# Kernel tuning notes

Hardware: AMD Instinct MI355X
Metric: run time of the kernel (lower is better)

Reference implementation:

```python
import math
import jax, jax.numpy as jnp
import numpy as np

B, T, D = 2, 2048, 1024
NUM_HEADS = 16
NUM_KV_HEADS = 4
HEAD_DIM = 64
ROPE_THETA = 500000.0


def precompute_freqs_cis(dim, seq_len, theta):
    freqs = 1.0 / theta ** (jnp.arange(0, dim, 2).astype(jnp.float32) / dim)
    freqs = jnp.outer(jnp.arange(seq_len), freqs)  # [T, dim//2]
    return jnp.cos(freqs), jnp.sin(freqs)


def apply_rotary_emb(xq, xk, cos, sin):
    # xq:[B,T,H,Dh], cos/sin:[T,Dh//2] -> broadcast as [1,T,1,Dh//2]
    c = cos[None, :, None, :]
    s = sin[None, :, None, :]

    def rot(x):
        xr = x.reshape(*x.shape[:-1], -1, 2)
        x0, x1 = xr[..., 0], xr[..., 1]
        return jnp.stack([x0 * c - x1 * s, x1 * c + x0 * s], axis=-1).reshape(x.shape)

    return rot(xq), rot(xk)


def setup_inputs() -> dict:
    key = jax.random.key(0)
    ks = jax.random.split(key, 5)
    x = jax.random.normal(ks[0], (B, T, D), dtype=jnp.float32)
    # causal mask [B,1,T,T]
    mask = jnp.broadcast_to(jnp.tril(jnp.ones((T, T), dtype=bool))[None, None], (B, 1, T, T))
    sq = 1.0 / math.sqrt(D)
    Wq = jax.random.normal(ks[1], (D, NUM_HEADS * HEAD_DIM), dtype=jnp.float32) * sq
    Wk = jax.random.normal(ks[2], (D, NUM_KV_HEADS * HEAD_DIM), dtype=jnp.float32) * sq
    Wv = jax.random.normal(ks[3], (D, NUM_KV_HEADS * HEAD_DIM), dtype=jnp.float32) * sq
    Wo = jax.random.normal(ks[4], (NUM_HEADS * HEAD_DIM, D), dtype=jnp.float32) * (1.0 / math.sqrt(NUM_HEADS * HEAD_DIM))
    return {"x": x, "mask": mask, "Wq": Wq, "Wk": Wk, "Wv": Wv, "Wo": Wo}


def reference(x, mask, Wq, Wk, Wv, Wo):
    b, t, _ = x.shape
    n_rep = NUM_HEADS // NUM_KV_HEADS
    q = (x @ Wq).reshape(b, t, NUM_HEADS, HEAD_DIM)
    k = (x @ Wk).reshape(b, t, NUM_KV_HEADS, HEAD_DIM)
    v = (x @ Wv).reshape(b, t, NUM_KV_HEADS, HEAD_DIM)
    cos, sin = precompute_freqs_cis(HEAD_DIM, t, ROPE_THETA)
    q, k = apply_rotary_emb(q, k, cos, sin)
    k = jnp.repeat(k, n_rep, axis=2)
    v = jnp.repeat(v, n_rep, axis=2)
    q = q.transpose(0, 2, 1, 3)  # [B,H,T,Dh]
    k = k.transpose(0, 2, 1, 3)
    v = v.transpose(0, 2, 1, 3)
    scale = 1.0 / math.sqrt(HEAD_DIM)
    attn = jnp.einsum('bhqd,bhkd->bhqk', q, k) * scale
    attn = jnp.where(mask, attn, -1e9)
    attn = jax.nn.softmax(attn, axis=-1)
    out = jnp.einsum('bhqk,bhkd->bhqd', attn, v)
    out = out.transpose(0, 2, 1, 3).reshape(b, t, -1)
    return out @ Wo
```

## Files before the change

### kernel.cpp

```cpp
#include <hip/hip_runtime.h>
#include <hip/hip_bf16.h>

#define B_  2
#define T_  2048
#define D_  1024
#define H_  16
#define KH_ 4
#define DH_ 64

typedef __attribute__((ext_vector_type(8))) short bf16x8;
typedef __attribute__((ext_vector_type(4))) float f32x4;

#define QSCALE 0.18033688011112043f

#if defined(__has_builtin)
#  if __has_builtin(__builtin_amdgcn_exp2f)
#    define EXP2F(x) __builtin_amdgcn_exp2f(x)
#  endif
#endif
#ifndef EXP2F
#  define EXP2F(x) exp2f(x)
#endif

__device__ __forceinline__ unsigned short f2bf(float f) {
  union { float f; unsigned int u; } v; v.f = f;
  return (unsigned short)((v.u + 0x7FFFu + ((v.u >> 16) & 1u)) >> 16);
}
__device__ __forceinline__ unsigned int pk2(float a, float b) {
  union { __hip_bfloat162 h2; unsigned int u; } v;
  v.h2 = __float22bfloat162_rn(make_float2(a, b));
  return v.u;
}

__device__ __forceinline__ void g2l16(const void* g, void* l) {
  __builtin_amdgcn_global_load_lds(
      (const __attribute__((address_space(1))) void*)g,
      (__attribute__((address_space(3))) void*)l, 16, 0, 0);
}


__global__ __launch_bounds__(256) void prep_kernel(
    const float* __restrict__ x,  const float* __restrict__ Wq,
    const float* __restrict__ Wk, const float* __restrict__ Wv,
    const float* __restrict__ Wo,
    short* __restrict__ xb, short* __restrict__ WT, short* __restrict__ WoT,
    float2* __restrict__ tbl) {
  __shared__ short Ts[64 * 72];
  const int bid = blockIdx.x, tid = threadIdx.x;

  if (bid < 2048) {
    const size_t i8 = ((size_t)bid * 256 + tid) * 8;
    const float4 a = *(const float4*)&x[i8];
    const float4 b = *(const float4*)&x[i8 + 4];
    uint4 p; p.x = pk2(a.x, a.y); p.y = pk2(a.z, a.w);
    p.z = pk2(b.x, b.y); p.w = pk2(b.z, b.w);
    *(uint4*)&xb[i8] = p;
  } else if (bid < 2688) {
    const bool isW = bid < 2432;
    const int idx = isW ? (bid - 2048) : (bid - 2432);
    const int n0 = (idx >> 4) * 64, k0 = (idx & 15) * 64;
    const float* src; int ncols, c0; short* dst;
    if (isW) {
      dst = WT;
      if (n0 < 1024)      { src = Wq; ncols = 1024; c0 = n0; }
      else if (n0 < 1280) { src = Wk; ncols = 256;  c0 = n0 - 1024; }
      else                { src = Wv; ncols = 256;  c0 = n0 - 1280; }
    } else { dst = WoT; src = Wo; ncols = 1024; c0 = n0; }
    for (int i = tid; i < 1024; i += 256) {
      const int kr = i >> 4, c4 = (i & 15) << 2;
      const int kc = isW ? kr : ((kr & 15) * 4 + (kr >> 4));
      const float4 w = *(const float4*)&src[(size_t)(k0 + kr) * ncols + c0 + c4];
      Ts[(c4 + 0) * 72 + kc] = (short)f2bf(w.x);
      Ts[(c4 + 1) * 72 + kc] = (short)f2bf(w.y);
      Ts[(c4 + 2) * 72 + kc] = (short)f2bf(w.z);
      Ts[(c4 + 3) * 72 + kc] = (short)f2bf(w.w);
    }
    __syncthreads();
    for (int c = tid; c < 512; c += 256) {
      const int nr = c >> 3, c8 = (c & 7) * 8;
      *(bf16x8*)&dst[(size_t)(n0 + nr) * 1024 + k0 + c8] =
          *(const bf16x8*)&Ts[nr * 72 + c8];
    }
  } else {
    const int e = (bid - 2688) * 256 + tid;
    const int t = e >> 5, i2 = e & 31;
    const float freq = exp2f(-(float)(2 * i2) * (18.931568569324174f / 64.0f));
    float sn, cs; sincosf((float)t * freq, &sn, &cs);
    tbl[e] = make_float2(cs, sn);
  }
}

__global__ __launch_bounds__(256) void qkv_mfma_kernel(
    const short* __restrict__ xb, const short* __restrict__ WT,
    const float2* __restrict__ tbl,
    short* __restrict__ qo, short* __restrict__ ko, short* __restrict__ vt) {
  __shared__ short Xsh[2][128 * 64];
  __shared__ short Wth[2][64 * 64];
  const int tid = threadIdx.x;
  const int lane = tid & 63, w = tid >> 6;
  const int lm = lane & 15, quad = lane >> 4;
  const int bid = blockIdx.x;
  const int xcd = bid & 7, slot = bid >> 3;
  const int m0 = (xcd * 4 + (slot & 3)) * 128;
  const int n0 = (slot >> 2) * 64;

  f32x4 acc[2][4];
  #pragma unroll
  for (int sm = 0; sm < 2; ++sm)
    #pragma unroll
    for (int ct = 0; ct < 4; ++ct) acc[sm][ct] = (f32x4){0.f, 0.f, 0.f, 0.f};

  auto stage = [&](int kt, int bsel) {
    #pragma unroll
    for (int u = 0; u < 4; ++u) {
      const int r = u * 32 + w * 8 + (lane >> 3);
      const int sb = (lane & 7) ^ (r & 7);
      g2l16(&xb[(size_t)(m0 + r) * 1024 + kt * 64 + sb * 8],
            &Xsh[bsel][(u * 32 + w * 8) * 64]);
    }
    #pragma unroll
    for (int u = 0; u < 2; ++u) {
      const int r = u * 32 + w * 8 + (lane >> 3);
      const int sb = (lane & 7) ^ (r & 7);
      g2l16(&WT[(size_t)(n0 + r) * 1024 + kt * 64 + sb * 8],
            &Wth[bsel][(u * 32 + w * 8) * 64]);
    }
  };

  stage(0, 0);
  for (int kt = 0; kt < 16; ++kt) {
    const int bsel = kt & 1;
    if (kt < 15) {
      stage(kt + 1, bsel ^ 1);
      asm volatile("s_waitcnt vmcnt(6)" ::: "memory");
    } else {
      asm volatile("s_waitcnt vmcnt(0)" ::: "memory");
    }
    __builtin_amdgcn_s_barrier();
    __builtin_amdgcn_sched_barrier(0);
    #pragma unroll
    for (int s2 = 0; s2 < 2; ++s2) {
      bf16x8 bfr[4];
      #pragma unroll
      for (int ct = 0; ct < 4; ++ct)
        bfr[ct] = *(const bf16x8*)&Wth[bsel][(ct * 16 + lm) * 64 +
                                            (((s2 * 4 + quad) ^ (lm & 7)) << 3)];
      #pragma unroll
      for (int sm = 0; sm < 2; ++sm) {
        const bf16x8 a = *(const bf16x8*)&Xsh[bsel][(w * 32 + sm * 16 + lm) * 64 +
                                            (((s2 * 4 + quad) ^ (lm & 7)) << 3)];
        #pragma unroll
        for (int ct = 0; ct < 4; ++ct)
          acc[sm][ct] =
              __builtin_amdgcn_mfma_f32_16x16x32_bf16(a, bfr[ct], acc[sm][ct], 0, 0, 0);
      }
    }
    __builtin_amdgcn_sched_barrier(0);
    __builtin_amdgcn_s_barrier();
  }

  if (n0 < 1280) {
    const bool isQ = n0 < 1024;
    short* outp = isQ ? qo : ko;
    const int base = isQ ? n0 : n0 - 1024;
    const int nh = isQ ? H_ : KH_;
    const int hh = base >> 6;
    const float post = isQ ? QSCALE : 1.0f;
    #pragma unroll
    for (int sm = 0; sm < 2; ++sm)
      #pragma unroll
      for (int r = 0; r < 4; ++r) {
        const int row = m0 + w * 32 + sm * 16 + quad * 4 + r;
        const int b = row >> 11, t = row & 2047;
        float v4[4];
        #pragma unroll
        for (int ct = 0; ct < 4; ++ct) {
          float val = acc[sm][ct][r];
          const float other = __shfl_xor(val, 1);
          const int ci = ct * 16 + lm;
          const float2 cs = tbl[t * 32 + (ci >> 1)];
          val = ((ci & 1) == 0) ? (val * cs.x - other * cs.y)
                                : (val * cs.x + other * cs.y);
          v4[ct] = val * post;
        }
        uint2 st; st.x = pk2(v4[0], v4[1]); st.y = pk2(v4[2], v4[3]);
        *(uint2*)&outp[((size_t)(b * nh + hh) * T_ + t) * DH_ + lm * 4] = st;
      }
  } else {
    short* XsF = &Xsh[0][0];
    __syncthreads();
    #pragma unroll
    for (int sm = 0; sm < 2; ++sm)
      #pragma unroll
      for (int r = 0; r < 4; ++r)
        #pragma unroll
        for (int ct = 0; ct < 4; ++ct)
          XsF[(w * 32 + sm * 16 + quad * 4 + r) * 72 + ct * 16 + lm] =
              (short)f2bf(acc[sm][ct][r]);
    __syncthreads();
    const int kh = (n0 - 1280) >> 6;
    const int b = m0 >> 11, t0 = m0 & 2047;
    short* vb = vt + (size_t)(b * KH_ + kh) * DH_ * T_;
    for (int c = tid; c < 1024; c += 256) {
      const int d = c >> 4, c8 = (c & 15) * 8;
      short tmp[8];
      #pragma unroll
      for (int j = 0; j < 8; ++j) {
        const int s = c8 + j, sg = s & 63;
        const int tok = (s & 64) | (sg & 35) | (((sg >> 2) & 1) << 4) |
                        (((sg >> 3) & 3) << 2);
        tmp[j] = XsF[tok * 72 + d];
      }
      *(bf16x8*)&vb[(size_t)d * T_ + t0 + c8] = *(bf16x8*)tmp;
    }
  }
}

__global__ __launch_bounds__(256, 4) void attn_mfma_kernel(
    const short* __restrict__ q, const short* __restrict__ k,
    const short* __restrict__ vt, short* __restrict__ att) {
  __shared__ short Ks[128 * 72];
  __shared__ short Vts[64 * 136];

  const int bx = blockIdx.x;
  const int jj = bx & 255, c2 = bx >> 8;
  int qt = (c2 & 1) ? (jj >> 3) : (31 - (jj >> 3));
  const int hb = (jj & 7) | (c2 << 3);
  const int h = hb >> 1, b = hb & 1;
  const int kh = h >> 2;
  const int tid = threadIdx.x;
  const int lane = tid & 63, w = tid >> 6;
  const int lm = lane & 15, quad = lane >> 4;
  const int q0 = qt * 64;

  const short* qb = q + (size_t)(b * H_ + h) * T_ * DH_;
  const short* kb = k + (size_t)(b * KH_ + kh) * T_ * DH_;
  const short* vb = vt + (size_t)(b * KH_ + kh) * DH_ * T_;

  bf16x8 ones;
  #pragma unroll
  for (int i = 0; i < 8; ++i) ones[i] = (short)0x3F80;

  bf16x8 aq[2];
  #pragma unroll
  for (int s = 0; s < 2; ++s)
    aq[s] = *(const bf16x8*)&qb[(size_t)(q0 + w * 16 + lm) * 64 + s * 32 + quad * 8];

  bf16x8 pk[4], pv[4];
  #pragma unroll
  for (int u = 0; u < 4; ++u) {
    const int c = tid + u * 256;
    const int row = c >> 3, c8 = (c & 7) * 8;
    pk[u] = *(const bf16x8*)&kb[(size_t)row * 64 + c8];
    const int d = c >> 4, c16 = (c & 15) * 8;
    pv[u] = *(const bf16x8*)&vb[(size_t)d * T_ + c16];
  }

  f32x4 oacc[4], lacc;
  #pragma unroll
  for (int i = 0; i < 4; ++i) oacc[i] = (f32x4){0.f, 0.f, 0.f, 0.f};
  lacc = (f32x4){0.f, 0.f, 0.f, 0.f};

  auto pairstep = [&](bool diag1) {
    f32x4 sacc0[4], sacc1[4];
    #pragma unroll
    for (int i = 0; i < 4; ++i) {
      sacc0[i] = (f32x4){0.f, 0.f, 0.f, 0.f};
      sacc1[i] = (f32x4){0.f, 0.f, 0.f, 0.f};
    }
    __builtin_amdgcn_s_setprio(1);
    #pragma unroll
    for (int s2 = 0; s2 < 2; ++s2)
      #pragma unroll
      for (int ct = 0; ct < 4; ++ct) {
        const bf16x8 bb =
            *(const bf16x8*)&Ks[(ct * 16 + lm) * 72 + s2 * 32 + quad * 8];
        sacc0[ct] = __builtin_amdgcn_mfma_f32_16x16x32_bf16(bb, aq[s2], sacc0[ct], 0, 0, 0);
      }
    #pragma unroll
    for (int s2 = 0; s2 < 2; ++s2)
      #pragma unroll
      for (int ct = 0; ct < 4; ++ct) {
        if (diag1 && ct > w) continue;
        const bf16x8 bb =
            *(const bf16x8*)&Ks[(64 + ct * 16 + lm) * 72 + s2 * 32 + quad * 8];
        sacc1[ct] = __builtin_amdgcn_mfma_f32_16x16x32_bf16(bb, aq[s2], sacc1[ct], 0, 0, 0);
      }
    __builtin_amdgcn_s_setprio(0);
    unsigned int pd0[4][2];
    #pragma unroll
    for (int ct = 0; ct < 4; ++ct) {
      float p[4];
      #pragma unroll
      for (int r = 0; r < 4; ++r) p[r] = EXP2F(sacc0[ct][r]);
      pd0[ct][0] = pk2(p[0], p[1]); pd0[ct][1] = pk2(p[2], p[3]);
    }
    __builtin_amdgcn_s_setprio(1);
    #pragma unroll
    for (int s2 = 0; s2 < 2; ++s2) {
      union { bf16x8 v; unsigned int u[4]; } pa;
      pa.u[0] = pd0[2 * s2][0];     pa.u[1] = pd0[2 * s2][1];
      pa.u[2] = pd0[2 * s2 + 1][0]; pa.u[3] = pd0[2 * s2 + 1][1];
      lacc = __builtin_amdgcn_mfma_f32_16x16x32_bf16(pa.v, ones, lacc, 0, 0, 0);
      #pragma unroll
      for (int ct = 0; ct < 4; ++ct) {
        const bf16x8 vfr = *(const bf16x8*)&Vts[(ct * 16 + lm) * 136 +
                                                s2 * 32 + quad * 8];
        oacc[ct] = __builtin_amdgcn_mfma_f32_16x16x32_bf16(pa.v, vfr, oacc[ct], 0, 0, 0);
      }
    }
    __builtin_amdgcn_s_setprio(0);
    unsigned int pd1[4][2];
    #pragma unroll
    for (int ct = 0; ct < 4; ++ct) {
      float p[4];
      #pragma unroll
      for (int r = 0; r < 4; ++r) {
        float e;
        if (diag1 && ct > w) e = 0.f;
        else {
          e = EXP2F(sacc1[ct][r]);
          if (diag1 && ct == w && (quad * 4 + r) > lm) e = 0.f;
        }
        p[r] = e;
      }
      pd1[ct][0] = pk2(p[0], p[1]); pd1[ct][1] = pk2(p[2], p[3]);
    }
    __builtin_amdgcn_s_setprio(1);
    #pragma unroll
    for (int s2 = 0; s2 < 2; ++s2) {
      if (diag1 && 2 * s2 > w) continue;
      union { bf16x8 v; unsigned int u[4]; } pa;
      pa.u[0] = pd1[2 * s2][0];     pa.u[1] = pd1[2 * s2][1];
      pa.u[2] = pd1[2 * s2 + 1][0]; pa.u[3] = pd1[2 * s2 + 1][1];
      lacc = __builtin_amdgcn_mfma_f32_16x16x32_bf16(pa.v, ones, lacc, 0, 0, 0);
      #pragma unroll
      for (int ct = 0; ct < 4; ++ct) {
        const bf16x8 vfr = *(const bf16x8*)&Vts[(ct * 16 + lm) * 136 +
                                                64 + s2 * 32 + quad * 8];
        oacc[ct] = __builtin_amdgcn_mfma_f32_16x16x32_bf16(pa.v, vfr, oacc[ct], 0, 0, 0);
      }
    }
    __builtin_amdgcn_s_setprio(0);
  };

  auto dstep = [&]() {
    f32x4 sacc[4];
    #pragma unroll
    for (int i = 0; i < 4; ++i) sacc[i] = (f32x4){0.f, 0.f, 0.f, 0.f};
    __builtin_amdgcn_s_setprio(1);
    #pragma unroll
    for (int s2 = 0; s2 < 2; ++s2)
      #pragma unroll
      for (int ct = 0; ct < 4; ++ct) {
        if (ct > w) continue;
        const bf16x8 bb =
            *(const bf16x8*)&Ks[(ct * 16 + lm) * 72 + s2 * 32 + quad * 8];
        sacc[ct] = __builtin_amdgcn_mfma_f32_16x16x32_bf16(bb, aq[s2], sacc[ct], 0, 0, 0);
      }
    __builtin_amdgcn_s_setprio(0);
    unsigned int pd[4][2];
    #pragma unroll
    for (int ct = 0; ct < 4; ++ct) {
      float p[4];
      #pragma unroll
      for (int r = 0; r < 4; ++r) {
        float e;
        if (ct > w) e = 0.f;
        else {
          e = EXP2F(sacc[ct][r]);
          if (ct == w && (quad * 4 + r) > lm) e = 0.f;
        }
        p[r] = e;
      }
      pd[ct][0] = pk2(p[0], p[1]); pd[ct][1] = pk2(p[2], p[3]);
    }
    __builtin_amdgcn_s_setprio(1);
    #pragma unroll
    for (int s2 = 0; s2 < 2; ++s2) {
      if (2 * s2 > w) continue;
      union { bf16x8 v; unsigned int u[4]; } pa;
      pa.u[0] = pd[2 * s2][0];     pa.u[1] = pd[2 * s2][1];
      pa.u[2] = pd[2 * s2 + 1][0]; pa.u[3] = pd[2 * s2 + 1][1];
      lacc = __builtin_amdgcn_mfma_f32_16x16x32_bf16(pa.v, ones, lacc, 0, 0, 0);
      #pragma unroll
      for (int ct = 0; ct < 4; ++ct) {
        const bf16x8 vfr = *(const bf16x8*)&Vts[(ct * 16 + lm) * 136 +
                                                s2 * 32 + quad * 8];
        oacc[ct] = __builtin_amdgcn_mfma_f32_16x16x32_bf16(pa.v, vfr, oacc[ct], 0, 0, 0);
      }
    }
    __builtin_amdgcn_s_setprio(0);
  };

  auto stage = [&](int r2) {
    __syncthreads();
    #pragma unroll
    for (int u = 0; u < 4; ++u) {
      const int c = tid + u * 256;
      const int row = c >> 3, c8 = (c & 7) * 8;
      *(bf16x8*)&Ks[row * 72 + c8] = pk[u];
      const int d = c >> 4, c16 = (c & 15) * 8;
      *(bf16x8*)&Vts[d * 136 + c16] = pv[u];
    }
    __syncthreads();
    const int r2n = (r2 + 2 <= qt) ? (r2 + 2) : r2;
    #pragma unroll
    for (int u = 0; u < 4; ++u) {
      const int c = tid + u * 256;
      const int row = c >> 3, c8 = (c & 7) * 8;
      pk[u] = *(const bf16x8*)&kb[(size_t)(r2n * 64 + row) * 64 + c8];
      const int d = c >> 4, c16 = (c & 15) * 8;
      pv[u] = *(const bf16x8*)&vb[(size_t)d * T_ + r2n * 64 + c16];
    }
  };

  int r2 = 0;
  for (; r2 + 1 <= qt; r2 += 2) {
    stage(r2);
    pairstep(r2 + 1 == qt);
  }
  if (r2 == qt) {
    stage(r2);
    dstep();
  }

  #pragma unroll
  for (int r = 0; r < 4; ++r) {
    const int qrow = q0 + w * 16 + quad * 4 + r;
    const float inv = 1.f / lacc[r];
    uint2 st;
    st.x = pk2(oacc[0][r] * inv, oacc[1][r] * inv);
    st.y = pk2(oacc[2][r] * inv, oacc[3][r] * inv);
    *(uint2*)&att[((size_t)b * T_ + qrow) * 1024 + h * 64 + lm * 4] = st;
  }
}

__global__ __launch_bounds__(256) void outproj_mfma_kernel(
    const short* __restrict__ att, const short* __restrict__ WoT,
    float* __restrict__ out) {
  __shared__ short Xsh[2][128 * 64];
  __shared__ short Wth[2][64 * 64];
  const int tid = threadIdx.x;
  const int lane = tid & 63, w = tid >> 6;
  const int lm = lane & 15, quad = lane >> 4;
  const int bid = blockIdx.x;
  const int xcd = bid & 7, slot = bid >> 3;
  const int m0 = (xcd * 4 + (slot & 3)) * 128;
  const int n0 = (slot >> 2) * 64;

  f32x4 acc[2][4];
  #pragma unroll
  for (int sm = 0; sm < 2; ++sm)
    #pragma unroll
    for (int ct = 0; ct < 4; ++ct) acc[sm][ct] = (f32x4){0.f, 0.f, 0.f, 0.f};

  auto stage = [&](int kt, int bsel) {
    #pragma unroll
    for (int u = 0; u < 4; ++u) {
      const int r = u * 32 + w * 8 + (lane >> 3);
      const int sb = (lane & 7) ^ (r & 7);
      g2l16(&att[(size_t)(m0 + r) * 1024 + kt * 64 + sb * 8],
            &Xsh[bsel][(u * 32 + w * 8) * 64]);
    }
    #pragma unroll
    for (int u = 0; u < 2; ++u) {
      const int r = u * 32 + w * 8 + (lane >> 3);
      const int sb = (lane & 7) ^ (r & 7);
      g2l16(&WoT[(size_t)(n0 + r) * 1024 + kt * 64 + sb * 8],
            &Wth[bsel][(u * 32 + w * 8) * 64]);
    }
  };

  stage(0, 0);
  for (int kt = 0; kt < 16; ++kt) {
    const int bsel = kt & 1;
    if (kt < 15) {
      stage(kt + 1, bsel ^ 1);
      asm volatile("s_waitcnt vmcnt(6)" ::: "memory");
    } else {
      asm volatile("s_waitcnt vmcnt(0)" ::: "memory");
    }
    __builtin_amdgcn_s_barrier();
    __builtin_amdgcn_sched_barrier(0);
    #pragma unroll
    for (int s2 = 0; s2 < 2; ++s2) {
      bf16x8 bfr[4];
      #pragma unroll
      for (int ct = 0; ct < 4; ++ct)
        bfr[ct] = *(const bf16x8*)&Wth[bsel][(ct * 16 + lm) * 64 +
                                            (((s2 * 4 + quad) ^ (lm & 7)) << 3)];
      #pragma unroll
      for (int sm = 0; sm < 2; ++sm) {
        const bf16x8 a = *(const bf16x8*)&Xsh[bsel][(w * 32 + sm * 16 + lm) * 64 +
                                            (((s2 * 4 + quad) ^ (lm & 7)) << 3)];
        #pragma unroll
        for (int ct = 0; ct < 4; ++ct)
          acc[sm][ct] =
              __builtin_amdgcn_mfma_f32_16x16x32_bf16(a, bfr[ct], acc[sm][ct], 0, 0, 0);
      }
    }
    __builtin_amdgcn_sched_barrier(0);
    __builtin_amdgcn_s_barrier();
  }

  #pragma unroll
  for (int sm = 0; sm < 2; ++sm)
    #pragma unroll
    for (int r = 0; r < 4; ++r) {
      const int row = m0 + w * 32 + sm * 16 + quad * 4 + r;
      #pragma unroll
      for (int ct = 0; ct < 4; ++ct)
        out[(size_t)row * 1024 + n0 + ct * 16 + lm] = acc[sm][ct][r];
    }
}

extern "C" void kernel_launch(void* const* d_in, const int* in_sizes, int n_in,
                              void* d_out, int out_size, void* d_ws, size_t ws_size,
                              hipStream_t stream) {
  const float* x  = (const float*)d_in[0];
  const float* Wq = (const float*)d_in[2];
  const float* Wk = (const float*)d_in[3];
  const float* Wv = (const float*)d_in[4];
  const float* Wo = (const float*)d_in[5];
  float* out = (float*)d_out;

  short* xb   = (short*)d_ws;
  short* WT   = xb  + (size_t)4194304;
  short* WoT  = WT  + (size_t)1572864;
  short* qb   = WoT + (size_t)1048576;
  short* kb   = qb  + (size_t)4194304;
  short* vtb  = kb  + (size_t)1048576;
  short* attb = vtb + (size_t)1048576;
  float2* tbl = (float2*)(attb + (size_t)4194304);

  prep_kernel<<<dim3(2944), dim3(256), 0, stream>>>(
      x, Wq, Wk, Wv, Wo, xb, WT, WoT, tbl);
  qkv_mfma_kernel<<<dim3(768), dim3(256), 0, stream>>>(xb, WT, tbl, qb, kb, vtb);
  attn_mfma_kernel<<<dim3(1024), dim3(256), 0, stream>>>(qb, kb, vtb, attb);
  outproj_mfma_kernel<<<dim3(512), dim3(256), 0, stream>>>(attb, WoT, out);
}
```

Before: 168.9 us.

## Split attention waves 2x2 over query and key halves with LDS reduction

The attention kernel's four waves are re-partitioned. Each wave now owns 32 query rows and half of each 64-key block, where before it owned 16 query rows and all keys. Each K and V fragment read from LDS now feeds two MFMA row tiles, which halves LDS traffic per MFMA, and causal diagonal work is spread more evenly across waves. The cost is a final cross-wave reduction of O and l through shared memory with an extra barrier, plus higher register pressure (doubled accumulators and Q fragments) under the 4-blocks-per-CU launch bound, which risks spills.

```diff
diff --git a/kernel.cpp b/kernel.cpp
--- a/kernel.cpp
+++ b/kernel.cpp
@@ -219,8 +219,9 @@
 __global__ __launch_bounds__(256, 4) void attn_mfma_kernel(
     const short* __restrict__ q, const short* __restrict__ k,
     const short* __restrict__ vt, short* __restrict__ att) {
-  __shared__ short Ks[128 * 72];
-  __shared__ short Vts[64 * 136];
+  __shared__ __align__(16) short SMEM[128 * 72 + 64 * 136];
+  short* Ks = SMEM;
+  short* Vts = SMEM + 128 * 72;
 
   const int bx = blockIdx.x;
   const int jj = bx & 255, c2 = bx >> 8;
@@ -230,6 +231,7 @@
   const int kh = h >> 2;
   const int tid = threadIdx.x;
   const int lane = tid & 63, w = tid >> 6;
+  const int wq = w >> 1, wk = w & 1;
   const int lm = lane & 15, quad = lane >> 4;
   const int q0 = qt * 64;
 
@@ -241,10 +243,13 @@
   #pragma unroll
   for (int i = 0; i < 8; ++i) ones[i] = (short)0x3F80;
 
-  bf16x8 aq[2];
-  #pragma unroll
-  for (int s = 0; s < 2; ++s)
-    aq[s] = *(const bf16x8*)&qb[(size_t)(q0 + w * 16 + lm) * 64 + s * 32 + quad * 8];
+  bf16x8 aq[2][2];
+  #pragma unroll
+  for (int sm = 0; sm < 2; ++sm)
+    #pragma unroll
+    for (int s2 = 0; s2 < 2; ++s2)
+      aq[sm][s2] = *(const bf16x8*)&qb[(size_t)(q0 + wq * 32 + sm * 16 + lm) * 64 +
+                                       s2 * 32 + quad * 8];
 
   bf16x8 pk[4], pv[4];
   #pragma unroll
@@ -256,139 +261,74 @@
     pv[u] = *(const bf16x8*)&vb[(size_t)d * T_ + c16];
   }
 
-  f32x4 oacc[4], lacc;
-  #pragma unroll
-  for (int i = 0; i < 4; ++i) oacc[i] = (f32x4){0.f, 0.f, 0.f, 0.f};
-  lacc = (f32x4){0.f, 0.f, 0.f, 0.f};
-
-  auto pairstep = [&](bool diag1) {
-    f32x4 sacc0[4], sacc1[4];
-    #pragma unroll
-    for (int i = 0; i < 4; ++i) {
-      sacc0[i] = (f32x4){0.f, 0.f, 0.f, 0.f};
-      sacc1[i] = (f32x4){0.f, 0.f, 0.f, 0.f};
-    }
+  f32x4 oacc[2][4], lacc[2];
+  #pragma unroll
+  for (int sm = 0; sm < 2; ++sm) {
+    #pragma unroll
+    for (int ct = 0; ct < 4; ++ct) oacc[sm][ct] = (f32x4){0.f, 0.f, 0.f, 0.f};
+    lacc[sm] = (f32x4){0.f, 0.f, 0.f, 0.f};
+  }
+
+  auto step = [&](int j, bool diag) {
+    f32x4 sacc[2][2];
+    #pragma unroll
+    for (int sm = 0; sm < 2; ++sm)
+      #pragma unroll
+      for (int ct2 = 0; ct2 < 2; ++ct2) sacc[sm][ct2] = (f32x4){0.f, 0.f, 0.f, 0.f};
     __builtin_amdgcn_s_setprio(1);
     #pragma unroll
-    for (int s2 = 0; s2 < 2; ++s2)
-      #pragma unroll
-      for (int ct = 0; ct < 4; ++ct) {
-        const bf16x8 bb =
-            *(const bf16x8*)&Ks[(ct * 16 + lm) * 72 + s2 * 32 + quad * 8];
-        sacc0[ct] = __builtin_amdgcn_mfma_f32_16x16x32_bf16(bb, aq[s2], sacc0[ct], 0, 0, 0);
-      }
-    #pragma unroll
-    for (int s2 = 0; s2 < 2; ++s2)
-      #pragma unroll
-      for (int ct = 0; ct < 4; ++ct) {
-        if (diag1 && ct > w) continue;
-        const bf16x8 bb =
-            *(const bf16x8*)&Ks[(64 + ct * 16 + lm) * 72 + s2 * 32 + quad * 8];
-        sacc1[ct] = __builtin_amdgcn_mfma_f32_16x16x32_bf16(bb, aq[s2], sacc1[ct], 0, 0, 0);
-      }
+    for (int s2 = 0; s2 < 2; ++s2) {
+      #pragma unroll
+      for (int ct2 = 0; ct2 < 2; ++ct2) {
+        const int kg = wk * 2 + ct2;
+        if (diag && kg > wq * 2 + 1) continue;
+        const bf16x8 bb = *(const bf16x8*)&Ks[(j * 64 + wk * 32 + ct2 * 16 + lm) * 72 +
+                                              s2 * 32 + quad * 8];
+        #pragma unroll
+        for (int sm = 0; sm < 2; ++sm) {
+          if (diag && kg > wq * 2 + sm) continue;
+          sacc[sm][ct2] =
+              __builtin_amdgcn_mfma_f32_16x16x32_bf16(bb, aq[sm][s2], sacc[sm][ct2], 0, 0, 0);
+        }
+      }
+    }
     __builtin_amdgcn_s_setprio(0);
-    unsigned int pd0[4][2];
-    #pragma unroll
-    for (int ct = 0; ct < 4; ++ct) {
-      float p[4];
-      #pragma unroll
-      for (int r = 0; r < 4; ++r) p[r] = EXP2F(sacc0[ct][r]);
-      pd0[ct][0] = pk2(p[0], p[1]); pd0[ct][1] = pk2(p[2], p[3]);
-    }
+    unsigned int pd[2][2][2];
+    #pragma unroll
+    for (int sm = 0; sm < 2; ++sm)
+      #pragma unroll
+      for (int ct2 = 0; ct2 < 2; ++ct2) {
+        const int kg = wk * 2 + ct2, qg = wq * 2 + sm;
+        float p[4];
+        #pragma unroll
+        for (int r = 0; r < 4; ++r) {
+          float e;
+          if (diag && kg > qg) e = 0.f;
+          else {
+            e = EXP2F(sacc[sm][ct2][r]);
+            if (diag && kg == qg && (quad * 4 + r) > lm) e = 0.f;
+          }
+          p[r] = e;
+        }
+        pd[sm][ct2][0] = pk2(p[0], p[1]);
+        pd[sm][ct2][1] = pk2(p[2], p[3]);
+      }
     __builtin_amdgcn_s_setprio(1);
-    #pragma unroll
-    for (int s2 = 0; s2 < 2; ++s2) {
+    bf16x8 vfr[4];
+    #pragma unroll
+    for (int ct = 0; ct < 4; ++ct)
+      vfr[ct] = *(const bf16x8*)&Vts[(ct * 16 + lm) * 136 + j * 64 + wk * 32 + quad * 8];
+    #pragma unroll
+    for (int sm = 0; sm < 2; ++sm) {
+      if (diag && wk * 2 > wq * 2 + sm) continue;
       union { bf16x8 v; unsigned int u[4]; } pa;
-      pa.u[0] = pd0[2 * s2][0];     pa.u[1] = pd0[2 * s2][1];
-      pa.u[2] = pd0[2 * s2 + 1][0]; pa.u[3] = pd0[2 * s2 + 1][1];
-      lacc = __builtin_amdgcn_mfma_f32_16x16x32_bf16(pa.v, ones, lacc, 0, 0, 0);
-      #pragma unroll
-      for (int ct = 0; ct < 4; ++ct) {
-        const bf16x8 vfr = *(const bf16x8*)&Vts[(ct * 16 + lm) * 136 +
-                                                s2 * 32 + quad * 8];
-        oacc[ct] = __builtin_amdgcn_mfma_f32_16x16x32_bf16(pa.v, vfr, oacc[ct], 0, 0, 0);
-      }
-    }
-    __builtin_amdgcn_s_setprio(0);
-    unsigned int pd1[4][2];
-    #pragma unroll
-    for (int ct = 0; ct < 4; ++ct) {
-      float p[4];
-      #pragma unroll
-      for (int r = 0; r < 4; ++r) {
-        float e;
-        if (diag1 && ct > w) e = 0.f;
-        else {
-          e = EXP2F(sacc1[ct][r]);
-          if (diag1 && ct == w && (quad * 4 + r) > lm) e = 0.f;
-        }
-        p[r] = e;
-      }
-      pd1[ct][0] = pk2(p[0], p[1]); pd1[ct][1] = pk2(p[2], p[3]);
-    }
-    __builtin_amdgcn_s_setprio(1);
-    #pragma unroll
-    for (int s2 = 0; s2 < 2; ++s2) {
-      if (diag1 && 2 * s2 > w) continue;
-      union { bf16x8 v; unsigned int u[4]; } pa;
-      pa.u[0] = pd1[2 * s2][0];     pa.u[1] = pd1[2 * s2][1];
-      pa.u[2] = pd1[2 * s2 + 1][0]; pa.u[3] = pd1[2 * s2 + 1][1];
-      lacc = __builtin_amdgcn_mfma_f32_16x16x32_bf16(pa.v, ones, lacc, 0, 0, 0);
-      #pragma unroll
-      for (int ct = 0; ct < 4; ++ct) {
-        const bf16x8 vfr = *(const bf16x8*)&Vts[(ct * 16 + lm) * 136 +
-                                                64 + s2 * 32 + quad * 8];
-        oacc[ct] = __builtin_amdgcn_mfma_f32_16x16x32_bf16(pa.v, vfr, oacc[ct], 0, 0, 0);
-      }
-    }
-    __builtin_amdgcn_s_setprio(0);
-  };
-
-  auto dstep = [&]() {
-    f32x4 sacc[4];
-    #pragma unroll
-    for (int i = 0; i < 4; ++i) sacc[i] = (f32x4){0.f, 0.f, 0.f, 0.f};
-    __builtin_amdgcn_s_setprio(1);
-    #pragma unroll
-    for (int s2 = 0; s2 < 2; ++s2)
-      #pragma unroll
-      for (int ct = 0; ct < 4; ++ct) {
-        if (ct > w) continue;
-        const bf16x8 bb =
-            *(const bf16x8*)&Ks[(ct * 16 + lm) * 72 + s2 * 32 + quad * 8];
-        sacc[ct] = __builtin_amdgcn_mfma_f32_16x16x32_bf16(bb, aq[s2], sacc[ct], 0, 0, 0);
-      }
-    __builtin_amdgcn_s_setprio(0);
-    unsigned int pd[4][2];
-    #pragma unroll
-    for (int ct = 0; ct < 4; ++ct) {
-      float p[4];
-      #pragma unroll
-      for (int r = 0; r < 4; ++r) {
-        float e;
-        if (ct > w) e = 0.f;
-        else {
-          e = EXP2F(sacc[ct][r]);
-          if (ct == w && (quad * 4 + r) > lm) e = 0.f;
-        }
-        p[r] = e;
-      }
-      pd[ct][0] = pk2(p[0], p[1]); pd[ct][1] = pk2(p[2], p[3]);
-    }
-    __builtin_amdgcn_s_setprio(1);
-    #pragma unroll
-    for (int s2 = 0; s2 < 2; ++s2) {
-      if (2 * s2 > w) continue;
-      union { bf16x8 v; unsigned int u[4]; } pa;
-      pa.u[0] = pd[2 * s2][0];     pa.u[1] = pd[2 * s2][1];
-      pa.u[2] = pd[2 * s2 + 1][0]; pa.u[3] = pd[2 * s2 + 1][1];
-      lacc = __builtin_amdgcn_mfma_f32_16x16x32_bf16(pa.v, ones, lacc, 0, 0, 0);
-      #pragma unroll
-      for (int ct = 0; ct < 4; ++ct) {
-        const bf16x8 vfr = *(const bf16x8*)&Vts[(ct * 16 + lm) * 136 +
-                                                s2 * 32 + quad * 8];
-        oacc[ct] = __builtin_amdgcn_mfma_f32_16x16x32_bf16(pa.v, vfr, oacc[ct], 0, 0, 0);
-      }
+      pa.u[0] = pd[sm][0][0]; pa.u[1] = pd[sm][0][1];
+      pa.u[2] = pd[sm][1][0]; pa.u[3] = pd[sm][1][1];
+      lacc[sm] = __builtin_amdgcn_mfma_f32_16x16x32_bf16(pa.v, ones, lacc[sm], 0, 0, 0);
+      #pragma unroll
+      for (int ct = 0; ct < 4; ++ct)
+        oacc[sm][ct] =
+            __builtin_amdgcn_mfma_f32_16x16x32_bf16(pa.v, vfr[ct], oacc[sm][ct], 0, 0, 0);
     }
     __builtin_amdgcn_s_setprio(0);
   };
@@ -418,21 +358,43 @@
   int r2 = 0;
   for (; r2 + 1 <= qt; r2 += 2) {
     stage(r2);
-    pairstep(r2 + 1 == qt);
+    step(0, false);
+    step(1, r2 + 1 == qt);
   }
   if (r2 == qt) {
     stage(r2);
-    dstep();
-  }
-
-  #pragma unroll
-  for (int r = 0; r < 4; ++r) {
-    const int qrow = q0 + w * 16 + quad * 4 + r;
-    const float inv = 1.f / lacc[r];
-    uint2 st;
-    st.x = pk2(oacc[0][r] * inv, oacc[1][r] * inv);
-    st.y = pk2(oacc[2][r] * inv, oacc[3][r] * inv);
-    *(uint2*)&att[((size_t)b * T_ + qrow) * 1024 + h * 64 + lm * 4] = st;
+    step(0, true);
+  }
+
+  __syncthreads();
+  float* LF = (float*)SMEM;
+  if (wk == 1) {
+    #pragma unroll
+    for (int sm = 0; sm < 2; ++sm) {
+      #pragma unroll
+      for (int ct = 0; ct < 4; ++ct)
+        *(f32x4*)&LF[(((wq * 2 + sm) * 4 + ct) * 64 + lane) * 4] = oacc[sm][ct];
+      *(f32x4*)&LF[4096 + ((wq * 2 + sm) * 64 + lane) * 4] = lacc[sm];
+    }
+  }
+  __syncthreads();
+  if (wk == 0) {
+    #pragma unroll
+    for (int sm = 0; sm < 2; ++sm) {
+      #pragma unroll
+      for (int ct = 0; ct < 4; ++ct)
+        oacc[sm][ct] += *(const f32x4*)&LF[(((wq * 2 + sm) * 4 + ct) * 64 + lane) * 4];
+      lacc[sm] += *(const f32x4*)&LF[4096 + ((wq * 2 + sm) * 64 + lane) * 4];
+      #pragma unroll
+      for (int r = 0; r < 4; ++r) {
+        const int qrow = q0 + wq * 32 + sm * 16 + quad * 4 + r;
+        const float inv = 1.f / lacc[sm][r];
+        uint2 st;
+        st.x = pk2(oacc[sm][0][r] * inv, oacc[sm][1][r] * inv);
+        st.y = pk2(oacc[sm][2][r] * inv, oacc[sm][3][r] * inv);
+        *(uint2*)&att[((size_t)b * T_ + qrow) * 1024 + h * 64 + lm * 4] = st;
+      }
+    }
   }
 }
 
```

Result: slower. 249.7 us (+47.8%).
